# Kernel optimization log

Hardware: AMD Instinct MI355X
Metric: run time of the kernel (lower is better)

## Reference

```python
import jax, jax.numpy as jnp
import numpy as np

N_NODES = 100000
N_EDGES = 1600000
N_GRAPHS = 64
FEAT = 64
EMB = 64
HID = 64
VOCAB = 32


def setup_inputs() -> dict:
    key = jax.random.key(0)
    ks = jax.random.split(key, 20)
    w = lambda k, sh: (jax.random.normal(k, sh, jnp.float32) * 0.05)
    x = jax.random.normal(ks[0], (N_NODES, FEAT), jnp.float32)
    edge_index = jax.random.randint(ks[1], (2, N_EDGES), 0, N_NODES, dtype=jnp.int32).astype(jnp.int64)
    batch = jnp.sort(jax.random.randint(ks[2], (N_NODES,), 0, N_GRAPHS, dtype=jnp.int32)).astype(jnp.int64)
    return {
        'x': x, 'edge_index': edge_index, 'batch': batch,
        # RGCN layer 1 (single relation): relation weight, root weight, bias
        'W1': w(ks[3], (FEAT, EMB)), 'root1': w(ks[4], (FEAT, EMB)), 'b1': w(ks[5], (EMB,)),
        # RGCN layer 2
        'W2': w(ks[6], (EMB, HID)), 'root2': w(ks[7], (EMB, HID)), 'b2': w(ks[8], (HID,)),
        # init_h / init_c linear heads
        'Wh': w(ks[9], (HID, HID)), 'bh': w(ks[10], (HID,)),
        'Wc': w(ks[11], (HID, HID)), 'bc': w(ks[12], (HID,)),
        # output layer
        'Wo': w(ks[13], (HID, VOCAB)), 'bo': w(ks[14], (VOCAB,)),
    }


def _rgcn(x, edge_index, W, root, b):
    # PyG RGCNConv with num_relations=1, aggr='mean':
    # out[i] = mean_{j in N(i)} (x[j] @ W) + x[i] @ root + b
    src, dst = edge_index[0], edge_index[1]
    msg = x[src] @ W                                    # [E, out] gather + small GEMM
    agg = jax.ops.segment_sum(msg, dst, num_segments=x.shape[0])
    cnt = jax.ops.segment_sum(jnp.ones((edge_index.shape[1],), x.dtype), dst, num_segments=x.shape[0])
    agg = agg / jnp.maximum(cnt, 1.0)[:, None]
    return agg + x @ root + b


def reference(x, edge_index, batch, W1, root1, b1, W2, root2, b2, Wh, bh, Wc, bc, Wo, bo):
    h = jax.nn.relu(_rgcn(x, edge_index, W1, root1, b1))
    h = jax.nn.relu(_rgcn(h, edge_index, W2, root2, b2))
    # global_mean_pool over graph-assignment vector `batch`
    summ = jax.ops.segment_sum(h, batch, num_segments=N_GRAPHS)
    cnt = jax.ops.segment_sum(jnp.ones((h.shape[0],), h.dtype), batch, num_segments=N_GRAPHS)
    pooled = summ / jnp.maximum(cnt, 1.0)[:, None]      # [G, HID]
    hidden = pooled @ Wh + bh
    cell = pooled @ Wc + bc
    logits = jax.nn.log_softmax(hidden @ Wo + bo, axis=1)
    return (logits, hidden, cell)
```

## Files before the change

### kernel.cpp

```cpp
#include <hip/hip_runtime.h>
#include <hip/hip_bf16.h>


typedef __attribute__((ext_vector_type(8))) short short8;
typedef __attribute__((ext_vector_type(4))) float f32x4;

#define RB 9
#define MAXBINS 256
#define CAP 12288
#define BCAP 14336
#define CHUNK 8192

__device__ inline float bf2f(unsigned short h) {
    return __uint_as_float(((unsigned int)h) << 16);
}
__device__ inline float bflo(unsigned int u) { return __uint_as_float(u << 16); }
__device__ inline float bfhi(unsigned int u) { return __uint_as_float(u & 0xffff0000u); }
__device__ inline unsigned short f2bf(float f) {
    unsigned int u = __float_as_uint(f);
    u = (u + 0x7fffu + ((u >> 16) & 1u)) >> 16;
    return (unsigned short)u;
}

__global__ __launch_bounds__(256) void prep_all(const float* __restrict__ x,
                                                unsigned short* __restrict__ xb, int n4,
                                                const float* __restrict__ W1,
                                                const float* __restrict__ R1,
                                                const float* __restrict__ W2,
                                                const float* __restrict__ R2,
                                                unsigned short* __restrict__ bt) {
    if (blockIdx.x < 2) {
        const float* W = blockIdx.x ? W2 : W1;
        const float* R = blockIdx.x ? R2 : R1;
        unsigned short* o = bt + (size_t)blockIdx.x * 8192;
        for (int idx = threadIdx.x; idx < 8192; idx += 256) {
            const int n = idx >> 6, k = idx & 63;
            const float v = (n < 64) ? W[k * 64 + n] : R[k * 64 + (n - 64)];
            o[idx] = f2bf(v);
        }
        return;
    }
    const int i = (blockIdx.x - 2) * 256 + threadIdx.x;
    if (i < n4) {
        const float4 v = ((const float4*)x)[i];
        ushort4 o;
        o.x = f2bf(v.x); o.y = f2bf(v.y); o.z = f2bf(v.z); o.w = f2bf(v.w);
        ((ushort4*)xb)[i] = o;
    }
}

__global__ __launch_bounds__(256) void bin_edges(const int* __restrict__ src,
                                                 const int* __restrict__ dst,
                                                 unsigned int* __restrict__ coarse,
                                                 int* __restrict__ gcur,
                                                 int E, int BINS) {
    __shared__ int cnt[MAXBINS];
    __shared__ int incl[MAXBINS];
    __shared__ int bstart[MAXBINS];
    __shared__ int bcur[MAXBINS];
    __shared__ int gbase[MAXBINS];
    __shared__ unsigned int stage[CHUNK];
    __shared__ unsigned char binOf[CHUNK];

    const int tid = threadIdx.x;
    const int chunk0 = blockIdx.x * CHUNK;
    int myS[32], myD[32];
#pragma unroll
    for (int k = 0; k < 32; ++k) {
        const int idx = chunk0 + k * 256 + tid;
        if (idx < E) { myS[k] = src[idx]; myD[k] = dst[idx]; }
        else myD[k] = -1;
    }
    cnt[tid] = 0;
    __syncthreads();
#pragma unroll
    for (int k = 0; k < 32; ++k)
        if (myD[k] >= 0) atomicAdd(&cnt[myD[k] >> RB], 1);
    __syncthreads();
    incl[tid] = cnt[tid];
    __syncthreads();
    for (int off = 1; off < 256; off <<= 1) {
        int t = (tid >= off) ? incl[tid - off] : 0;
        __syncthreads();
        incl[tid] += t;
        __syncthreads();
    }
    bstart[tid] = incl[tid] - cnt[tid];
    bcur[tid] = incl[tid] - cnt[tid];
    __syncthreads();
#pragma unroll
    for (int k = 0; k < 32; ++k) {
        if (myD[k] >= 0) {
            const int b = myD[k] >> RB;
            const int pos = atomicAdd(&bcur[b], 1);
            stage[pos] = (unsigned int)myS[k] | ((unsigned int)(myD[k] & ((1 << RB) - 1)) << 17);
            binOf[pos] = (unsigned char)b;
        }
    }
    __syncthreads();
    if (tid < BINS && cnt[tid] > 0)
        gbase[tid] = tid * CAP + atomicAdd(&gcur[tid], cnt[tid]);
    __syncthreads();
    int total = E - chunk0;
    if (total > CHUNK) total = CHUNK;
    for (int idx = tid; idx < total; idx += 256) {
        const int b = binOf[idx];
        coarse[gbase[b] + (idx - bstart[b])] = stage[idx];
    }
}

__global__ __launch_bounds__(256) void finalize_csr(const unsigned int* __restrict__ coarse,
                                                    const int* __restrict__ gcur,
                                                    int* __restrict__ bucket,
                                                    int* __restrict__ pstart,
                                                    int* __restrict__ degarr,
                                                    int N, int BINS) {
    __shared__ int ncnt[512];
    __shared__ int pexcl[512];
    __shared__ int ncur[512];
    __shared__ int s2[256];
    __shared__ unsigned int st[BCAP];
    __shared__ int ptot;

    const int b = blockIdx.x;
    const int tid = threadIdx.x;
    const int cb = gcur[b];
    const int base = b * BCAP;
    const unsigned int* reg = coarse + (size_t)b * CAP;
    const int node0 = b << RB;
    int nloc = N - node0;
    if (nloc > 512) nloc = 512;

    ncnt[tid] = 0; ncnt[tid + 256] = 0;
    __syncthreads();
    for (int idx = tid; idx < cb; idx += 256)
        atomicAdd(&ncnt[reg[idx] >> 17], 1);
    __syncthreads();
    const int p0 = (ncnt[2 * tid] + 15) & ~15;
    const int p1 = (ncnt[2 * tid + 1] + 15) & ~15;
    s2[tid] = p0 + p1;
    __syncthreads();
    for (int off = 1; off < 256; off <<= 1) {
        int t = (tid >= off) ? s2[tid - off] : 0;
        __syncthreads();
        s2[tid] += t;
        __syncthreads();
    }
    const int pairExcl = s2[tid] - (p0 + p1);
    pexcl[2 * tid] = pairExcl;
    pexcl[2 * tid + 1] = pairExcl + p0;
    ncur[2 * tid] = pairExcl;
    ncur[2 * tid + 1] = pairExcl + p0;
    if (tid == 255) ptot = s2[255];
    __syncthreads();
    const int total = ptot;
    for (int idx = tid; idx < total; idx += 256) st[idx] = (unsigned int)N;
    for (int i = tid; i < nloc; i += 256) {
        pstart[node0 + i] = base + pexcl[i];
        degarr[node0 + i] = ncnt[i];
    }
    __syncthreads();
    for (int idx = tid; idx < cb; idx += 256) {
        const unsigned int e = reg[idx];
        const int p = atomicAdd(&ncur[e >> 17], 1);
        st[p] = e & 0x1FFFFu;
    }
    __syncthreads();
    for (int idx = tid; idx < total; idx += 256) bucket[base + idx] = (int)st[idx];
}

__global__ __launch_bounds__(256) void gemm_xwr(const unsigned short* __restrict__ xin,
                                                const unsigned short* __restrict__ bt,
                                                const float* __restrict__ bias,
                                                unsigned short* __restrict__ xw,
                                                unsigned short* __restrict__ xrb,
                                                int M) {
    if (blockIdx.x == 0 && threadIdx.x < 32)
        *(unsigned int*)&xw[(size_t)M * 64 + threadIdx.x * 2] = 0u;

    const int lane = threadIdx.x & 63;
    const int q = lane >> 4;
    const int mm = lane & 15;

    short8 bfrag[8][2];
#pragma unroll
    for (int t = 0; t < 8; ++t)
#pragma unroll
        for (int c = 0; c < 2; ++c)
            bfrag[t][c] = *(const short8*)&bt[(size_t)(t * 16 + mm) * 64 + c * 32 + q * 8];
    float bv[4];
#pragma unroll
    for (int tt = 0; tt < 4; ++tt) bv[tt] = bias[tt * 16 + mm];

    const int wid = threadIdx.x >> 6;
    const int gw = blockIdx.x * 4 + wid;
    const int nw = gridDim.x * 4;
    const int ntiles = M >> 4;

    for (int tile = gw; tile < ntiles; tile += nw) {
        const int row0 = tile << 4;
        const short8 a0 = *(const short8*)&xin[(size_t)(row0 + mm) * 64 + q * 8];
        const short8 a1 = *(const short8*)&xin[(size_t)(row0 + mm) * 64 + 32 + q * 8];
        f32x4 acc[8];
#pragma unroll
        for (int t = 0; t < 8; ++t) {
            acc[t] = (f32x4){0.f, 0.f, 0.f, 0.f};
            acc[t] = __builtin_amdgcn_mfma_f32_16x16x32_bf16(a0, bfrag[t][0], acc[t], 0, 0, 0);
            acc[t] = __builtin_amdgcn_mfma_f32_16x16x32_bf16(a1, bfrag[t][1], acc[t], 0, 0, 0);
        }
#pragma unroll
        for (int t = 0; t < 4; ++t) {
#pragma unroll
            for (int r = 0; r < 4; ++r) {
                const float v = acc[t][r];
                const float vn = __shfl_down(v, 1);
                if (!(mm & 1)) {
                    const unsigned int u = (unsigned int)f2bf(v) | ((unsigned int)f2bf(vn) << 16);
                    *(unsigned int*)&xw[(size_t)(row0 + q * 4 + r) * 64 + t * 16 + mm] = u;
                }
            }
        }
#pragma unroll
        for (int t = 4; t < 8; ++t) {
#pragma unroll
            for (int r = 0; r < 4; ++r) {
                const float v = acc[t][r] + bv[t - 4];
                const float vn = __shfl_down(v, 1);
                if (!(mm & 1)) {
                    const unsigned int u = (unsigned int)f2bf(v) | ((unsigned int)f2bf(vn) << 16);
                    *(unsigned int*)&xrb[(size_t)(row0 + q * 4 + r) * 64 + (t - 4) * 16 + mm] = u;
                }
            }
        }
    }
}

__global__ __launch_bounds__(256) void aggregate(const unsigned short* __restrict__ xw,
                                                 const unsigned short* __restrict__ xrb,
                                                 const int* __restrict__ pstart,
                                                 const int* __restrict__ degarr,
                                                 const int* __restrict__ bucket,
                                                 unsigned short* __restrict__ outb,
                                                 int N) {
    const int lane = threadIdx.x & 63;
    const int half = lane >> 5;
    const int fl = lane & 31;
    const int wid = threadIdx.x >> 6;
    const int gw = blockIdx.x * 4 + wid;
    const int nw = gridDim.x * 4;

    for (int i = gw; i < N; i += nw) {
        const int r0 = pstart[i];
        const int dg = degarr[i];
        const int pdeg = (dg + 15) & ~15;
        float lo0 = 0.f, lo1 = 0.f, lo2 = 0.f, lo3 = 0.f;
        float hi0 = 0.f, hi1 = 0.f, hi2 = 0.f, hi3 = 0.f;
        for (int base = 0; base < pdeg; base += 64) {
            const int rem = pdeg - base;
            const int s = (lane < rem) ? bucket[r0 + base + lane] : N;
            const int mm = rem < 64 ? rem : 64;
            for (int t = 0; t < mm; t += 16) {
                unsigned int u[8];
#pragma unroll
                for (int p = 0; p < 8; ++p) {
                    const int rr = __shfl(s, t + 2 * p + half);
                    u[p] = *(const unsigned int*)&xw[(size_t)rr * 64 + fl * 2];
                }
                lo0 += bflo(u[0]); hi0 += bfhi(u[0]);
                lo1 += bflo(u[1]); hi1 += bfhi(u[1]);
                lo2 += bflo(u[2]); hi2 += bfhi(u[2]);
                lo3 += bflo(u[3]); hi3 += bfhi(u[3]);
                lo0 += bflo(u[4]); hi0 += bfhi(u[4]);
                lo1 += bflo(u[5]); hi1 += bfhi(u[5]);
                lo2 += bflo(u[6]); hi2 += bfhi(u[6]);
                lo3 += bflo(u[7]); hi3 += bfhi(u[7]);
            }
        }
        float lo = (lo0 + lo1) + (lo2 + lo3);
        float hi = (hi0 + hi1) + (hi2 + hi3);
        lo += __shfl_xor(lo, 32);
        hi += __shfl_xor(hi, 32);

        const float inv = 1.0f / (float)(dg > 0 ? dg : 1);
        const unsigned int ur = *(const unsigned int*)&xrb[(size_t)i * 64 + fl * 2];
        const float o0 = fmaxf(lo * inv + bflo(ur), 0.f);
        const float o1 = fmaxf(hi * inv + bfhi(ur), 0.f);
        if (half == 0) {
            const unsigned int u = (unsigned int)f2bf(o0) | ((unsigned int)f2bf(o1) << 16);
            *(unsigned int*)&outb[(size_t)i * 64 + fl * 2] = u;
        }
    }
}

__global__ __launch_bounds__(256) void pool_kernel(const unsigned short* __restrict__ h,
                                                   const int* __restrict__ batch,
                                                   float* __restrict__ pooled, int N) {
    __shared__ float red[16][64];
    __shared__ int bnds[2];
    const int gph = blockIdx.x;
    if (threadIdx.x < 2) {
        const int target = gph + threadIdx.x;
        int lo = 0, hi = N;
        while (lo < hi) {
            int mid = (lo + hi) >> 1;
            if (batch[mid] < target) lo = mid + 1; else hi = mid;
        }
        bnds[threadIdx.x] = lo;
    }
    __syncthreads();
    const int r0 = bnds[0], r1 = bnds[1];
    const int f = threadIdx.x & 15;
    const int r = threadIdx.x >> 4;
    float4 acc = {0.f, 0.f, 0.f, 0.f};
    for (int row = r0 + r; row < r1; row += 16) {
        const ushort4 v = *(const ushort4*)&h[(size_t)row * 64 + f * 4];
        acc.x += bf2f(v.x); acc.y += bf2f(v.y);
        acc.z += bf2f(v.z); acc.w += bf2f(v.w);
    }
    red[r][f * 4 + 0] = acc.x; red[r][f * 4 + 1] = acc.y;
    red[r][f * 4 + 2] = acc.z; red[r][f * 4 + 3] = acc.w;
    __syncthreads();
    if (threadIdx.x < 64) {
        float s = 0.f;
        for (int j = 0; j < 16; ++j) s += red[j][threadIdx.x];
        const int cnt = r1 - r0;
        const float invc = 1.0f / (float)(cnt > 0 ? cnt : 1);
        pooled[gph * 64 + threadIdx.x] = s * invc;
    }
}

__global__ __launch_bounds__(256) void head_kernel(const float* __restrict__ pooled,
                                                   const float* __restrict__ Wh,
                                                   const float* __restrict__ bh,
                                                   const float* __restrict__ Wc,
                                                   const float* __restrict__ bc,
                                                   const float* __restrict__ Wo,
                                                   const float* __restrict__ bo,
                                                   float* __restrict__ out) {
    __shared__ float pm[4096];
    __shared__ float hid[4096];
    __shared__ float lg[2048];
    const int t = threadIdx.x;

    for (int idx = t; idx < 4096; idx += 256) pm[idx] = pooled[idx];
    __syncthreads();

    for (int idx = t; idx < 4096; idx += 256) {
        int g = idx >> 6, o = idx & 63;
        float ah = bh[o], ac = bc[o];
        for (int k = 0; k < 64; ++k) {
            float p = pm[(g << 6) + k];
            ah += p * Wh[k * 64 + o];
            ac += p * Wc[k * 64 + o];
        }
        hid[idx] = ah;
        out[2048 + idx] = ah;
        out[6144 + idx] = ac;
    }
    __syncthreads();

    for (int idx = t; idx < 2048; idx += 256) {
        int g = idx >> 5, v = idx & 31;
        float a = bo[v];
        for (int k = 0; k < 64; ++k) a += hid[(g << 6) + k] * Wo[k * 32 + v];
        lg[idx] = a;
    }
    __syncthreads();

    if (t < 64) {
        float mx = -3.4e38f;
        for (int v = 0; v < 32; ++v) mx = fmaxf(mx, lg[(t << 5) + v]);
        float s = 0.f;
        for (int v = 0; v < 32; ++v) s += expf(lg[(t << 5) + v] - mx);
        float lse = mx + logf(s);
        for (int v = 0; v < 32; ++v) out[(t << 5) + v] = lg[(t << 5) + v] - lse;
    }
}

extern "C" void kernel_launch(void* const* d_in, const int* in_sizes, int n_in,
                              void* d_out, int out_size, void* d_ws, size_t ws_size,
                              hipStream_t stream) {
    const float* x = (const float*)d_in[0];
    const int* ei = (const int*)d_in[1];
    const int* batch = (const int*)d_in[2];
    const float* W1 = (const float*)d_in[3];
    const float* root1 = (const float*)d_in[4];
    const float* b1 = (const float*)d_in[5];
    const float* W2 = (const float*)d_in[6];
    const float* root2 = (const float*)d_in[7];
    const float* b2 = (const float*)d_in[8];
    const float* Wh = (const float*)d_in[9];
    const float* bh = (const float*)d_in[10];
    const float* Wc = (const float*)d_in[11];
    const float* bc = (const float*)d_in[12];
    const float* Wo = (const float*)d_in[13];
    const float* bo = (const float*)d_in[14];
    float* out = (float*)d_out;

    const int N = in_sizes[0] / 64;
    const int E = in_sizes[1] / 2;
    const int* srcp = ei;
    const int* dstp = ei + E;
    const int BINS = (N + (1 << RB) - 1) >> RB;

    char* ws = (char*)d_ws;
    size_t off = 0;
    auto alloc = [&](size_t bytes) -> void* {
        void* p = ws + off;
        off += (bytes + 255) & ~(size_t)255;
        return p;
    };
    int* pstart = (int*)alloc((size_t)N * 4);
    int* degarr = (int*)alloc((size_t)N * 4);
    int* bucket = (int*)alloc((size_t)BINS * BCAP * 4);
    unsigned short* xb = (unsigned short*)alloc((size_t)N * 64 * 2);
    unsigned short* h1 = (unsigned short*)alloc((size_t)N * 64 * 2);
    size_t xw_bytes = (size_t)(N + 1) * 64 * 2;
    size_t coarse_bytes = (size_t)BINS * CAP * 4;
    unsigned short* xw = (unsigned short*)alloc(xw_bytes > coarse_bytes ? xw_bytes : coarse_bytes);
    unsigned int* coarse = (unsigned int*)xw;
    unsigned short* xrb = (unsigned short*)alloc((size_t)N * 64 * 2);
    unsigned short* bt = (unsigned short*)alloc(2 * 8192 * 2);
    float* pooled = (float*)alloc(4096 * 4);
    int* gcur = (int*)alloc(MAXBINS * 4);
    unsigned short* h2 = xb;

    const int n4 = N * 16;
    const int nbBin = (E + CHUNK - 1) / CHUNK;

    hipMemsetAsync(gcur, 0, MAXBINS * 4, stream);
    bin_edges<<<nbBin, 256, 0, stream>>>(srcp, dstp, coarse, gcur, E, BINS);
    finalize_csr<<<BINS, 256, 0, stream>>>(coarse, gcur, bucket, pstart, degarr, N, BINS);

    prep_all<<<2 + (n4 + 255) / 256, 256, 0, stream>>>(x, xb, n4, W1, root1, W2, root2, bt);

    gemm_xwr<<<1024, 256, 0, stream>>>(xb, bt, b1, xw, xrb, N);
    aggregate<<<4096, 256, 0, stream>>>(xw, xrb, pstart, degarr, bucket, h1, N);
    gemm_xwr<<<1024, 256, 0, stream>>>(h1, bt + 8192, b2, xw, xrb, N);
    aggregate<<<4096, 256, 0, stream>>>(xw, xrb, pstart, degarr, bucket, h2, N);

    pool_kernel<<<64, 256, 0, stream>>>(h2, batch, pooled, N);
    head_kernel<<<1, 256, 0, stream>>>(pooled, Wh, bh, Wc, bc, Wo, bo, out);
}
```

Before: 298.2 us.

## Fuse CSR finalize with first GEMM and process two nodes per wave in aggregate

```diff
diff --git a/kernel.cpp b/kernel.cpp
--- a/kernel.cpp
+++ b/kernel.cpp
@@ -22,38 +22,16 @@
     return (unsigned short)u;
 }
 
-__global__ __launch_bounds__(256) void prep_all(const float* __restrict__ x,
-                                                unsigned short* __restrict__ xb, int n4,
+__global__ __launch_bounds__(256) void bin_prep(const int* __restrict__ src,
+                                                const int* __restrict__ dst,
+                                                unsigned int* __restrict__ coarse,
+                                                int* __restrict__ gcur,
+                                                int E, int BINS, int nbBin,
                                                 const float* __restrict__ W1,
                                                 const float* __restrict__ R1,
                                                 const float* __restrict__ W2,
                                                 const float* __restrict__ R2,
                                                 unsigned short* __restrict__ bt) {
-    if (blockIdx.x < 2) {
-        const float* W = blockIdx.x ? W2 : W1;
-        const float* R = blockIdx.x ? R2 : R1;
-        unsigned short* o = bt + (size_t)blockIdx.x * 8192;
-        for (int idx = threadIdx.x; idx < 8192; idx += 256) {
-            const int n = idx >> 6, k = idx & 63;
-            const float v = (n < 64) ? W[k * 64 + n] : R[k * 64 + (n - 64)];
-            o[idx] = f2bf(v);
-        }
-        return;
-    }
-    const int i = (blockIdx.x - 2) * 256 + threadIdx.x;
-    if (i < n4) {
-        const float4 v = ((const float4*)x)[i];
-        ushort4 o;
-        o.x = f2bf(v.x); o.y = f2bf(v.y); o.z = f2bf(v.z); o.w = f2bf(v.w);
-        ((ushort4*)xb)[i] = o;
-    }
-}
-
-__global__ __launch_bounds__(256) void bin_edges(const int* __restrict__ src,
-                                                 const int* __restrict__ dst,
-                                                 unsigned int* __restrict__ coarse,
-                                                 int* __restrict__ gcur,
-                                                 int E, int BINS) {
     __shared__ int cnt[MAXBINS];
     __shared__ int incl[MAXBINS];
     __shared__ int bstart[MAXBINS];
@@ -63,6 +41,19 @@
     __shared__ unsigned char binOf[CHUNK];
 
     const int tid = threadIdx.x;
+    if (blockIdx.x >= nbBin) {
+        const int layer = blockIdx.x - nbBin;
+        const float* W = layer ? W2 : W1;
+        const float* R = layer ? R2 : R1;
+        unsigned short* o = bt + (size_t)layer * 8192;
+        for (int idx = tid; idx < 8192; idx += 256) {
+            const int n = idx >> 6, k = idx & 63;
+            const float v = (n < 64) ? W[k * 64 + n] : R[k * 64 + (n - 64)];
+            o[idx] = f2bf(v);
+        }
+        return;
+    }
+
     const int chunk0 = blockIdx.x * CHUNK;
     int myS[32], myD[32];
 #pragma unroll
@@ -109,64 +100,141 @@
     }
 }
 
-__global__ __launch_bounds__(256) void finalize_csr(const unsigned int* __restrict__ coarse,
-                                                    const int* __restrict__ gcur,
-                                                    int* __restrict__ bucket,
-                                                    int* __restrict__ pstart,
-                                                    int* __restrict__ degarr,
-                                                    int N, int BINS) {
+__global__ __launch_bounds__(256) void fin_gemm1(const unsigned int* __restrict__ coarse,
+                                                 const int* __restrict__ gcur,
+                                                 int* __restrict__ bucket,
+                                                 int* __restrict__ pstart,
+                                                 int* __restrict__ degarr,
+                                                 int N, int BINS,
+                                                 const float* __restrict__ x,
+                                                 const unsigned short* __restrict__ bt,
+                                                 const float* __restrict__ bias,
+                                                 unsigned short* __restrict__ xw,
+                                                 unsigned short* __restrict__ xrb) {
     __shared__ int ncnt[512];
     __shared__ int pexcl[512];
     __shared__ int ncur[512];
     __shared__ int s2[256];
-    __shared__ unsigned int st[BCAP];
     __shared__ int ptot;
 
-    const int b = blockIdx.x;
     const int tid = threadIdx.x;
-    const int cb = gcur[b];
-    const int base = b * BCAP;
-    const unsigned int* reg = coarse + (size_t)b * CAP;
-    const int node0 = b << RB;
-    int nloc = N - node0;
-    if (nloc > 512) nloc = 512;
-
-    ncnt[tid] = 0; ncnt[tid + 256] = 0;
-    __syncthreads();
-    for (int idx = tid; idx < cb; idx += 256)
-        atomicAdd(&ncnt[reg[idx] >> 17], 1);
-    __syncthreads();
-    const int p0 = (ncnt[2 * tid] + 15) & ~15;
-    const int p1 = (ncnt[2 * tid + 1] + 15) & ~15;
-    s2[tid] = p0 + p1;
-    __syncthreads();
-    for (int off = 1; off < 256; off <<= 1) {
-        int t = (tid >= off) ? s2[tid - off] : 0;
-        __syncthreads();
-        s2[tid] += t;
-        __syncthreads();
-    }
-    const int pairExcl = s2[tid] - (p0 + p1);
-    pexcl[2 * tid] = pairExcl;
-    pexcl[2 * tid + 1] = pairExcl + p0;
-    ncur[2 * tid] = pairExcl;
-    ncur[2 * tid + 1] = pairExcl + p0;
-    if (tid == 255) ptot = s2[255];
-    __syncthreads();
-    const int total = ptot;
-    for (int idx = tid; idx < total; idx += 256) st[idx] = (unsigned int)N;
-    for (int i = tid; i < nloc; i += 256) {
-        pstart[node0 + i] = base + pexcl[i];
-        degarr[node0 + i] = ncnt[i];
-    }
-    __syncthreads();
-    for (int idx = tid; idx < cb; idx += 256) {
-        const unsigned int e = reg[idx];
-        const int p = atomicAdd(&ncur[e >> 17], 1);
-        st[p] = e & 0x1FFFFu;
-    }
-    __syncthreads();
-    for (int idx = tid; idx < total; idx += 256) bucket[base + idx] = (int)st[idx];
+    if (blockIdx.x < (unsigned)BINS) {
+        const int b = blockIdx.x;
+        const int cb = gcur[b];
+        const int base = b * BCAP;
+        const unsigned int* reg = coarse + (size_t)b * CAP;
+        const int node0 = b << RB;
+        int nloc = N - node0;
+        if (nloc > 512) nloc = 512;
+
+        ncnt[tid] = 0; ncnt[tid + 256] = 0;
+        __syncthreads();
+        for (int idx = tid; idx < cb; idx += 256)
+            atomicAdd(&ncnt[reg[idx] >> 17], 1);
+        __syncthreads();
+        const int p0 = (ncnt[2 * tid] + 15) & ~15;
+        const int p1 = (ncnt[2 * tid + 1] + 15) & ~15;
+        s2[tid] = p0 + p1;
+        __syncthreads();
+        for (int off = 1; off < 256; off <<= 1) {
+            int t = (tid >= off) ? s2[tid - off] : 0;
+            __syncthreads();
+            s2[tid] += t;
+            __syncthreads();
+        }
+        const int pairExcl = s2[tid] - (p0 + p1);
+        pexcl[2 * tid] = pairExcl;
+        pexcl[2 * tid + 1] = pairExcl + p0;
+        ncur[2 * tid] = pairExcl;
+        ncur[2 * tid + 1] = pairExcl + p0;
+        if (tid == 255) ptot = s2[255];
+        __syncthreads();
+        const int total = ptot;
+        for (int i = tid; i < nloc; i += 256) {
+            pstart[node0 + i] = base + pexcl[i];
+            degarr[node0 + i] = ncnt[i];
+        }
+        for (int idx = tid; idx < total; idx += 256) bucket[base + idx] = N;
+        __syncthreads();
+        for (int idx = tid; idx < cb; idx += 256) {
+            const unsigned int e = reg[idx];
+            const int p = atomicAdd(&ncur[e >> 17], 1);
+            bucket[base + p] = (int)(e & 0x1FFFFu);
+        }
+        return;
+    }
+
+    const int gb = blockIdx.x - BINS;
+    if (gb == 0 && tid < 32)
+        *(unsigned int*)&xw[(size_t)N * 64 + tid * 2] = 0u;
+
+    const int lane = tid & 63;
+    const int q = lane >> 4;
+    const int mm = lane & 15;
+
+    short8 bfrag[8][2];
+#pragma unroll
+    for (int t = 0; t < 8; ++t)
+#pragma unroll
+        for (int c = 0; c < 2; ++c)
+            bfrag[t][c] = *(const short8*)&bt[(size_t)(t * 16 + mm) * 64 + c * 32 + q * 8];
+    float bv[4];
+#pragma unroll
+    for (int tt = 0; tt < 4; ++tt) bv[tt] = bias[tt * 16 + mm];
+
+    const int wid = tid >> 6;
+    const int gw = gb * 4 + wid;
+    const int nw = 1024 * 4;
+    const int ntiles = N >> 4;
+
+    for (int tile = gw; tile < ntiles; tile += nw) {
+        const int row0 = tile << 4;
+        const float* ap = &x[(size_t)(row0 + mm) * 64 + q * 8];
+        const float4 f0 = *(const float4*)ap;
+        const float4 f1 = *(const float4*)(ap + 4);
+        const float4 f2 = *(const float4*)(ap + 32);
+        const float4 f3 = *(const float4*)(ap + 36);
+        short8 a0, a1;
+        a0[0] = (short)f2bf(f0.x); a0[1] = (short)f2bf(f0.y);
+        a0[2] = (short)f2bf(f0.z); a0[3] = (short)f2bf(f0.w);
+        a0[4] = (short)f2bf(f1.x); a0[5] = (short)f2bf(f1.y);
+        a0[6] = (short)f2bf(f1.z); a0[7] = (short)f2bf(f1.w);
+        a1[0] = (short)f2bf(f2.x); a1[1] = (short)f2bf(f2.y);
+        a1[2] = (short)f2bf(f2.z); a1[3] = (short)f2bf(f2.w);
+        a1[4] = (short)f2bf(f3.x); a1[5] = (short)f2bf(f3.y);
+        a1[6] = (short)f2bf(f3.z); a1[7] = (short)f2bf(f3.w);
+        f32x4 acc[8];
+#pragma unroll
+        for (int t = 0; t < 8; ++t) {
+            acc[t] = (f32x4){0.f, 0.f, 0.f, 0.f};
+            acc[t] = __builtin_amdgcn_mfma_f32_16x16x32_bf16(a0, bfrag[t][0], acc[t], 0, 0, 0);
+            acc[t] = __builtin_amdgcn_mfma_f32_16x16x32_bf16(a1, bfrag[t][1], acc[t], 0, 0, 0);
+        }
+#pragma unroll
+        for (int t = 0; t < 4; ++t) {
+#pragma unroll
+            for (int r = 0; r < 4; ++r) {
+                const float v = acc[t][r];
+                const float vn = __shfl_down(v, 1);
+                if (!(mm & 1)) {
+                    const unsigned int u = (unsigned int)f2bf(v) | ((unsigned int)f2bf(vn) << 16);
+                    *(unsigned int*)&xw[(size_t)(row0 + q * 4 + r) * 64 + t * 16 + mm] = u;
+                }
+            }
+        }
+#pragma unroll
+        for (int t = 4; t < 8; ++t) {
+#pragma unroll
+            for (int r = 0; r < 4; ++r) {
+                const float v = acc[t][r] + bv[t - 4];
+                const float vn = __shfl_down(v, 1);
+                if (!(mm & 1)) {
+                    const unsigned int u = (unsigned int)f2bf(v) | ((unsigned int)f2bf(vn) << 16);
+                    *(unsigned int*)&xrb[(size_t)(row0 + q * 4 + r) * 64 + (t - 4) * 16 + mm] = u;
+                }
+            }
+        }
+    }
 }
 
 __global__ __launch_bounds__(256) void gemm_xwr(const unsigned short* __restrict__ xin,
@@ -232,6 +300,28 @@
                 }
             }
         }
+    }
+}
+
+__device__ inline void agg_steps(const unsigned short* __restrict__ xw, int s, int t0, int t1,
+                                 int half, int fl,
+                                 float& l0, float& l1, float& l2, float& l3,
+                                 float& h0, float& h1, float& h2, float& h3) {
+    for (int t = t0; t < t1; t += 16) {
+        unsigned int u[8];
+#pragma unroll
+        for (int p = 0; p < 8; ++p) {
+            const int rr = __shfl(s, t + 2 * p + half);
+            u[p] = *(const unsigned int*)&xw[(size_t)rr * 64 + fl * 2];
+        }
+        l0 += bflo(u[0]); h0 += bfhi(u[0]);
+        l1 += bflo(u[1]); h1 += bfhi(u[1]);
+        l2 += bflo(u[2]); h2 += bfhi(u[2]);
+        l3 += bflo(u[3]); h3 += bfhi(u[3]);
+        l0 += bflo(u[4]); h0 += bfhi(u[4]);
+        l1 += bflo(u[5]); h1 += bfhi(u[5]);
+        l2 += bflo(u[6]); h2 += bfhi(u[6]);
+        l3 += bflo(u[7]); h3 += bfhi(u[7]);
     }
 }
 
@@ -249,45 +339,96 @@
     const int gw = blockIdx.x * 4 + wid;
     const int nw = gridDim.x * 4;
 
-    for (int i = gw; i < N; i += nw) {
-        const int r0 = pstart[i];
-        const int dg = degarr[i];
-        const int pdeg = (dg + 15) & ~15;
-        float lo0 = 0.f, lo1 = 0.f, lo2 = 0.f, lo3 = 0.f;
-        float hi0 = 0.f, hi1 = 0.f, hi2 = 0.f, hi3 = 0.f;
-        for (int base = 0; base < pdeg; base += 64) {
-            const int rem = pdeg - base;
-            const int s = (lane < rem) ? bucket[r0 + base + lane] : N;
-            const int mm = rem < 64 ? rem : 64;
-            for (int t = 0; t < mm; t += 16) {
-                unsigned int u[8];
-#pragma unroll
-                for (int p = 0; p < 8; ++p) {
-                    const int rr = __shfl(s, t + 2 * p + half);
-                    u[p] = *(const unsigned int*)&xw[(size_t)rr * 64 + fl * 2];
-                }
-                lo0 += bflo(u[0]); hi0 += bfhi(u[0]);
-                lo1 += bflo(u[1]); hi1 += bfhi(u[1]);
-                lo2 += bflo(u[2]); hi2 += bfhi(u[2]);
-                lo3 += bflo(u[3]); hi3 += bfhi(u[3]);
-                lo0 += bflo(u[4]); hi0 += bfhi(u[4]);
-                lo1 += bflo(u[5]); hi1 += bfhi(u[5]);
-                lo2 += bflo(u[6]); hi2 += bfhi(u[6]);
-                lo3 += bflo(u[7]); hi3 += bfhi(u[7]);
-            }
-        }
-        float lo = (lo0 + lo1) + (lo2 + lo3);
-        float hi = (hi0 + hi1) + (hi2 + hi3);
-        lo += __shfl_xor(lo, 32);
-        hi += __shfl_xor(hi, 32);
-
-        const float inv = 1.0f / (float)(dg > 0 ? dg : 1);
-        const unsigned int ur = *(const unsigned int*)&xrb[(size_t)i * 64 + fl * 2];
-        const float o0 = fmaxf(lo * inv + bflo(ur), 0.f);
-        const float o1 = fmaxf(hi * inv + bfhi(ur), 0.f);
-        if (half == 0) {
+    for (int i = gw; i < N; i += 2 * nw) {
+        const int iB = i + nw;
+        const int hasB = (iB < N);
+        const int r0A = pstart[i];
+        const int dgA = degarr[i];
+        const int r0B = hasB ? pstart[iB] : r0A;
+        const int dgB = hasB ? degarr[iB] : 0;
+        const int pA = (dgA + 15) & ~15;
+        const int pB = (dgB + 15) & ~15;
+
+        float lA0 = 0.f, lA1 = 0.f, lA2 = 0.f, lA3 = 0.f;
+        float hA0 = 0.f, hA1 = 0.f, hA2 = 0.f, hA3 = 0.f;
+        float lB0 = 0.f, lB1 = 0.f, lB2 = 0.f, lB3 = 0.f;
+        float hB0 = 0.f, hB1 = 0.f, hB2 = 0.f, hB3 = 0.f;
+
+        if (pA <= 64 && pB <= 64) {
+            const int sA = bucket[r0A + lane];
+            const int sB = bucket[r0B + lane];
+            const int pmax = pA > pB ? pA : pB;
+            for (int t = 0; t < pmax; t += 16) {
+                unsigned int uA[8], uB[8];
+                const bool doA = t < pA, doB = t < pB;
+                if (doA) {
+#pragma unroll
+                    for (int p = 0; p < 8; ++p) {
+                        const int rr = __shfl(sA, t + 2 * p + half);
+                        uA[p] = *(const unsigned int*)&xw[(size_t)rr * 64 + fl * 2];
+                    }
+                }
+                if (doB) {
+#pragma unroll
+                    for (int p = 0; p < 8; ++p) {
+                        const int rr = __shfl(sB, t + 2 * p + half);
+                        uB[p] = *(const unsigned int*)&xw[(size_t)rr * 64 + fl * 2];
+                    }
+                }
+                if (doA) {
+                    lA0 += bflo(uA[0]); hA0 += bfhi(uA[0]);
+                    lA1 += bflo(uA[1]); hA1 += bfhi(uA[1]);
+                    lA2 += bflo(uA[2]); hA2 += bfhi(uA[2]);
+                    lA3 += bflo(uA[3]); hA3 += bfhi(uA[3]);
+                    lA0 += bflo(uA[4]); hA0 += bfhi(uA[4]);
+                    lA1 += bflo(uA[5]); hA1 += bfhi(uA[5]);
+                    lA2 += bflo(uA[6]); hA2 += bfhi(uA[6]);
+                    lA3 += bflo(uA[7]); hA3 += bfhi(uA[7]);
+                }
+                if (doB) {
+                    lB0 += bflo(uB[0]); hB0 += bfhi(uB[0]);
+                    lB1 += bflo(uB[1]); hB1 += bfhi(uB[1]);
+                    lB2 += bflo(uB[2]); hB2 += bfhi(uB[2]);
+                    lB3 += bflo(uB[3]); hB3 += bfhi(uB[3]);
+                    lB0 += bflo(uB[4]); hB0 += bfhi(uB[4]);
+                    lB1 += bflo(uB[5]); hB1 += bfhi(uB[5]);
+                    lB2 += bflo(uB[6]); hB2 += bfhi(uB[6]);
+                    lB3 += bflo(uB[7]); hB3 += bfhi(uB[7]);
+                }
+            }
+        } else {
+            for (int base = 0; base < pA; base += 64) {
+                const int rem = pA - base;
+                const int s = (lane < rem) ? bucket[r0A + base + lane] : N;
+                const int mmx = rem < 64 ? rem : 64;
+                agg_steps(xw, s, 0, mmx, half, fl, lA0, lA1, lA2, lA3, hA0, hA1, hA2, hA3);
+            }
+            for (int base = 0; base < pB; base += 64) {
+                const int rem = pB - base;
+                const int s = (lane < rem) ? bucket[r0B + base + lane] : N;
+                const int mmx = rem < 64 ? rem : 64;
+                agg_steps(xw, s, 0, mmx, half, fl, lB0, lB1, lB2, lB3, hB0, hB1, hB2, hB3);
+            }
+        }
+
+        float loA = (lA0 + lA1) + (lA2 + lA3);
+        float hiA = (hA0 + hA1) + (hA2 + hA3);
+        float loB = (lB0 + lB1) + (lB2 + lB3);
+        float hiB = (hB0 + hB1) + (hB2 + hB3);
+        loA += __shfl_xor(loA, 32); hiA += __shfl_xor(hiA, 32);
+        loB += __shfl_xor(loB, 32); hiB += __shfl_xor(hiB, 32);
+
+        const float invA = 1.0f / (float)(dgA > 0 ? dgA : 1);
+        const float invB = 1.0f / (float)(dgB > 0 ? dgB : 1);
+        const int row = (hasB && half) ? iB : i;
+        const float mylo = half ? loB * invB : loA * invA;
+        const float myhi = half ? hiB * invB : hiA * invA;
+        const unsigned int ur = *(const unsigned int*)&xrb[(size_t)row * 64 + fl * 2];
+        const float o0 = fmaxf(mylo + bflo(ur), 0.f);
+        const float o1 = fmaxf(myhi + bfhi(ur), 0.f);
+        if (hasB || half == 0) {
             const unsigned int u = (unsigned int)f2bf(o0) | ((unsigned int)f2bf(o1) << 16);
-            *(unsigned int*)&outb[(size_t)i * 64 + fl * 2] = u;
+            *(unsigned int*)&outb[(size_t)row * 64 + fl * 2] = u;
         }
     }
 }
@@ -412,32 +553,26 @@
     };
     int* pstart = (int*)alloc((size_t)N * 4);
     int* degarr = (int*)alloc((size_t)N * 4);
-    int* bucket = (int*)alloc((size_t)BINS * BCAP * 4);
-    unsigned short* xb = (unsigned short*)alloc((size_t)N * 64 * 2);
+    int* bucket = (int*)alloc(((size_t)BINS * BCAP + 256) * 4);
+    unsigned int* coarse = (unsigned int*)alloc((size_t)BINS * CAP * 4);
     unsigned short* h1 = (unsigned short*)alloc((size_t)N * 64 * 2);
-    size_t xw_bytes = (size_t)(N + 1) * 64 * 2;
-    size_t coarse_bytes = (size_t)BINS * CAP * 4;
-    unsigned short* xw = (unsigned short*)alloc(xw_bytes > coarse_bytes ? xw_bytes : coarse_bytes);
-    unsigned int* coarse = (unsigned int*)xw;
+    unsigned short* h2 = (unsigned short*)alloc((size_t)N * 64 * 2);
+    unsigned short* xw = (unsigned short*)alloc((size_t)(N + 1) * 64 * 2);
     unsigned short* xrb = (unsigned short*)alloc((size_t)N * 64 * 2);
     unsigned short* bt = (unsigned short*)alloc(2 * 8192 * 2);
     float* pooled = (float*)alloc(4096 * 4);
     int* gcur = (int*)alloc(MAXBINS * 4);
-    unsigned short* h2 = xb;
-
-    const int n4 = N * 16;
+
     const int nbBin = (E + CHUNK - 1) / CHUNK;
 
     hipMemsetAsync(gcur, 0, MAXBINS * 4, stream);
-    bin_edges<<<nbBin, 256, 0, stream>>>(srcp, dstp, coarse, gcur, E, BINS);
-    finalize_csr<<<BINS, 256, 0, stream>>>(coarse, gcur, bucket, pstart, degarr, N, BINS);
-
-    prep_all<<<2 + (n4 + 255) / 256, 256, 0, stream>>>(x, xb, n4, W1, root1, W2, root2, bt);
-
-    gemm_xwr<<<1024, 256, 0, stream>>>(xb, bt, b1, xw, xrb, N);
-    aggregate<<<4096, 256, 0, stream>>>(xw, xrb, pstart, degarr, bucket, h1, N);
+    bin_prep<<<nbBin + 2, 256, 0, stream>>>(srcp, dstp, coarse, gcur, E, BINS, nbBin,
+                                            W1, root1, W2, root2, bt);
+    fin_gemm1<<<BINS + 1024, 256, 0, stream>>>(coarse, gcur, bucket, pstart, degarr, N, BINS,
+                                               x, bt, b1, xw, xrb);
+    aggregate<<<2048, 256, 0, stream>>>(xw, xrb, pstart, degarr, bucket, h1, N);
     gemm_xwr<<<1024, 256, 0, stream>>>(h1, bt + 8192, b2, xw, xrb, N);
-    aggregate<<<4096, 256, 0, stream>>>(xw, xrb, pstart, degarr, bucket, h2, N);
+    aggregate<<<2048, 256, 0, stream>>>(xw, xrb, pstart, degarr, bucket, h2, N);
 
     pool_kernel<<<64, 256, 0, stream>>>(h2, batch, pooled, N);
     head_kernel<<<1, 256, 0, stream>>>(pooled, Wh, bh, Wc, bc, Wo, bo, out);
```

After: 301.9 us. No clear change (+1.3%).
